# Optimization experiments

Measured on AMD Instinct MI355X. Metric: run time of the kernel, lower is better.

The kernel has to match this reference:

```python
import jax, jax.numpy as jnp
import numpy as np

D_MODEL = 1024
N_HEADS = 16
HEAD_DIM = D_MODEL // N_HEADS
ROPE_BASE = 10000.0


def _rope_cos_sin(t, dtype):
    # inv_freq over half the head dim, standard RoPE (GPT-NeoX style)
    inv_freq = 1.0 / (ROPE_BASE ** (jnp.arange(0, HEAD_DIM, 2, dtype=jnp.float32) / HEAD_DIM))
    freqs = jnp.arange(t, dtype=jnp.float32)[:, None] * inv_freq[None, :]  # [t, hd/2]
    emb = jnp.concatenate([freqs, freqs], axis=-1)  # [t, hd]
    return jnp.cos(emb).astype(dtype), jnp.sin(emb).astype(dtype)


def _rotate_half(x):
    x1, x2 = jnp.split(x, 2, axis=-1)
    return jnp.concatenate([-x2, x1], axis=-1)


def _apply_rope(x, cos, sin):
    # x: [b, h, t, hd]; cos/sin: [t, hd]
    return x * cos[None, None] + _rotate_half(x) * sin[None, None]


def setup_inputs() -> dict:
    key = jax.random.key(0)
    kx, kqkv, kout = jax.random.split(key, 3)
    x = jax.random.normal(kx, (4, 2048, D_MODEL), dtype=jnp.float32)
    scale = 1.0 / np.sqrt(D_MODEL)
    Wqkv = jax.random.normal(kqkv, (D_MODEL, 3 * D_MODEL), dtype=jnp.float32) * scale
    Wout = jax.random.normal(kout, (D_MODEL, D_MODEL), dtype=jnp.float32) * scale
    return {"x": x, "Wqkv": Wqkv, "Wout": Wout}


def reference(x, Wqkv, Wout):
    b, t, _ = x.shape
    qkv = (x @ Wqkv).reshape(b, t, 3, N_HEADS, HEAD_DIM)
    q, k, v = qkv[:, :, 0], qkv[:, :, 1], qkv[:, :, 2]  # [b, t, h, hd]
    q = q.transpose(0, 2, 1, 3)  # [b, h, t, hd]
    k = k.transpose(0, 2, 1, 3)
    v = v.transpose(0, 2, 1, 3)
    cos, sin = _rope_cos_sin(t, x.dtype)
    q = _apply_rope(q, cos, sin)
    k = _apply_rope(k, cos, sin)
    # causal SDPA
    scores = jnp.einsum("bhqd,bhkd->bhqk", q, k) / np.sqrt(HEAD_DIM)
    causal = jnp.tril(jnp.ones((t, t), dtype=bool))
    scores = jnp.where(causal[None, None], scores, jnp.finfo(scores.dtype).min)
    attn = jax.nn.softmax(scores, axis=-1)
    out = jnp.einsum("bhqk,bhkd->bhqd", attn, v)
    out = out.transpose(0, 2, 1, 3).reshape(b, t, D_MODEL)
    return out @ Wout
```

## Files before the change

### kernel.cpp

```cpp
#include <hip/hip_runtime.h>
#include <cstdint>
#include <cstddef>

typedef __bf16 bf16;
typedef __bf16 bf16x8 __attribute__((ext_vector_type(8)));
typedef __bf16 bf16x4 __attribute__((ext_vector_type(4)));
typedef float  f32x4  __attribute__((ext_vector_type(4)));
typedef float  f32x16 __attribute__((ext_vector_type(16)));

#define MFMA16(a, b, c) __builtin_amdgcn_mfma_f32_16x16x32_bf16((a), (b), (c), 0, 0, 0)
#define MFMA32(a, b, c) __builtin_amdgcn_mfma_f32_32x32x16_bf16((a), (b), (c), 0, 0, 0)

static constexpr int BB   = 4;
static constexpr int TT   = 2048;
static constexpr int DM   = 1024;
static constexpr int NH   = 16;
static constexpr int HD   = 64;
static constexpr int TOK  = BB * TT;
static constexpr int NQKV = 3 * DM;

__device__ inline void gload16(const void* g, void* l) {
    __builtin_amdgcn_global_load_lds((const __attribute__((address_space(1))) void*)g,
                                     (__attribute__((address_space(3))) void*)l, 16, 0, 0);
}

__device__ inline int swz(int x) { return x ^ ((x >> 3) & 0x70); }

__global__ void k_cvt(const float* __restrict__ in, bf16* __restrict__ out, int n) {
    int i = (blockIdx.x * blockDim.x + threadIdx.x) * 4;
    if (i >= n) return;
    float4 v = *(const float4*)(in + i);
    bf16x4 o;
    o[0] = (bf16)v.x; o[1] = (bf16)v.y; o[2] = (bf16)v.z; o[3] = (bf16)v.w;
    *(bf16x4*)(out + i) = o;
}

__global__ void k_transpose_cvt(const float* __restrict__ in, bf16* __restrict__ out,
                                int R, int C) {
    __shared__ bf16 tl[64 * 72];
    int tid = threadIdx.x;
    int c0 = blockIdx.x * 64, r0 = blockIdx.y * 64;
#pragma unroll
    for (int rep = 0; rep < 4; rep++) {
        int r = rep * 16 + (tid >> 4);
        int c = (tid & 15) * 4;
        float4 v = *(const float4*)(in + (size_t)(r0 + r) * C + c0 + c);
        tl[r * 72 + c + 0] = (bf16)v.x;
        tl[r * 72 + c + 1] = (bf16)v.y;
        tl[r * 72 + c + 2] = (bf16)v.z;
        tl[r * 72 + c + 3] = (bf16)v.w;
    }
    __syncthreads();
#pragma unroll
    for (int rep = 0; rep < 4; rep++) {
        int cc = rep * 16 + (tid >> 4);
        int rr = (tid & 15) * 4;
        bf16x4 o;
        o[0] = tl[(rr + 0) * 72 + cc];
        o[1] = tl[(rr + 1) * 72 + cc];
        o[2] = tl[(rr + 2) * 72 + cc];
        o[3] = tl[(rr + 3) * 72 + cc];
        *(bf16x4*)(out + (size_t)(c0 + cc) * R + r0 + rr) = o;
    }
}

__global__ void k_rope_tab(float* __restrict__ ct, float* __restrict__ st) {
    int i = blockIdx.x * blockDim.x + threadIdx.x;
    int t = i >> 5, j = i & 31;
    float invf = powf(10000.0f, -(float)j * (1.0f / 32.0f));
    float a = (float)t * invf;
    ct[i] = cosf(a);
    st[i] = sinf(a);
}

template <int MODE>
__global__ __launch_bounds__(256) void k_gemm_bt(
    const bf16* __restrict__ A, const bf16* __restrict__ Bt,
    int M, int N, int K,
    float* __restrict__ outF,
    bf16* __restrict__ qbuf, bf16* __restrict__ kbuf, bf16* __restrict__ vbuf,
    const float* __restrict__ ct, const float* __restrict__ st, float qscale) {
    __shared__ bf16 lA[128 * 64];
    __shared__ bf16 lB[128 * 64];
    int tid = threadIdx.x;
    int l = tid & 63, wid = tid >> 6;
    int wm = wid >> 1, wn = wid & 1;
    int bn = blockIdx.x, bm = blockIdx.y;
    const bf16* Ab = A + (size_t)bm * 128 * K;
    const bf16* Bb = Bt + (size_t)bn * 128 * K;
    int srow = l >> 3, scol = (l & 7) * 8;
    f32x4 acc[4][4] = {};
    for (int kt = 0; kt < K; kt += 64) {
        __syncthreads();
#pragma unroll
        for (int i = 0; i < 4; i++) {
            int chunk = wid * 4 + i;
            gload16(Ab + (size_t)(chunk * 8 + srow) * K + kt + scol, &lA[chunk * 512]);
            gload16(Bb + (size_t)(chunk * 8 + srow) * K + kt + scol, &lB[chunk * 512]);
        }
        __syncthreads();
#pragma unroll
        for (int kk = 0; kk < 2; kk++) {
            bf16x8 af[4], bfr[4];
#pragma unroll
            for (int mi = 0; mi < 4; mi++)
                af[mi] = *(const bf16x8*)&lA[(wm * 64 + mi * 16 + (l & 15)) * 64 + kk * 32 + (l >> 4) * 8];
#pragma unroll
            for (int ni = 0; ni < 4; ni++)
                bfr[ni] = *(const bf16x8*)&lB[(wn * 64 + ni * 16 + (l & 15)) * 64 + kk * 32 + (l >> 4) * 8];
#pragma unroll
            for (int mi = 0; mi < 4; mi++)
#pragma unroll
                for (int ni = 0; ni < 4; ni++)
                    acc[mi][ni] = MFMA16(af[mi], bfr[ni], acc[mi][ni]);
        }
    }
    if (MODE == 2) {
#pragma unroll
        for (int mi = 0; mi < 4; mi++) {
            int m0 = bm * 128 + wm * 64 + mi * 16 + ((l >> 4) << 2);
#pragma unroll
            for (int ni = 0; ni < 4; ni++) {
                int n = bn * 128 + wn * 64 + ni * 16 + (l & 15);
#pragma unroll
                for (int rj = 0; rj < 4; rj++)
                    outF[(size_t)(m0 + rj) * N + n] = acc[mi][ni][rj];
            }
        }
    } else {
        int n0 = bn * 128 + wn * 64;
        int sQ = n0 >> 10;
        int h = (n0 & 1023) >> 6;
        if (sQ == 2) {
#pragma unroll
            for (int ni = 0; ni < 4; ni++) {
                int d = ni * 16 + (l & 15);
#pragma unroll
                for (int mi = 0; mi < 4; mi++) {
                    int m0 = bm * 128 + wm * 64 + mi * 16 + ((l >> 4) << 2);
                    int b = m0 >> 11, t0 = m0 & 2047;
                    bf16x4 pv;
#pragma unroll
                    for (int rj = 0; rj < 4; rj++) pv[rj] = (bf16)acc[mi][ni][rj];
                    *(bf16x4*)(vbuf + ((size_t)((b * NH + h) * HD + d)) * TT + t0) = pv;
                }
            }
        } else {
            float qs = (sQ == 0) ? qscale : 1.0f;
            bf16* obuf = (sQ == 0) ? qbuf : kbuf;
#pragma unroll
            for (int mi = 0; mi < 4; mi++) {
                int m0 = bm * 128 + wm * 64 + mi * 16 + ((l >> 4) << 2);
                int b = m0 >> 11, t0 = m0 & 2047;
#pragma unroll
                for (int rj = 0; rj < 4; rj++) {
                    int t = t0 + rj;
                    bf16* dst = obuf + ((size_t)(b * NH + h) * TT + t) * HD;
                    const float* crow = ct + t * 32;
                    const float* srow = st + t * 32;
#pragma unroll
                    for (int ni2 = 0; ni2 < 2; ni2++) {
                        int d = ni2 * 16 + (l & 15);
                        float cs = crow[d], sn = srow[d];
                        float a  = acc[mi][ni2][rj];
                        float b2 = acc[mi][ni2 + 2][rj];
                        dst[d]      = (bf16)(qs * (a  * cs - b2 * sn));
                        dst[d + 32] = (bf16)(qs * (b2 * cs + a  * sn));
                    }
                }
            }
        }
    }
}

__global__ __launch_bounds__(256, 2) void k_attn(
    const bf16* __restrict__ Q, const bf16* __restrict__ K,
    const bf16* __restrict__ Vt, bf16* __restrict__ O) {
    __shared__ bf16 lK[2][4096];
    __shared__ bf16 lV[2][4096];
    __shared__ bf16 lP[8192];
    int tid = threadIdx.x;
    int l = tid & 63, w = tid >> 6;
    int bx = blockIdx.x, by = blockIdx.y;
    int bh = bx * 8 + (by >> 3);
    int p = by & 7;
    const char* KbB = (const char*)(K + (size_t)bh * TT * HD);
    const char* VbB = (const char*)(Vt + (size_t)bh * HD * TT);
    int b = bh >> 4, h = bh & 15;

    bf16x8 ones;
#pragma unroll
    for (int e = 0; e < 8; e++) ones[e] = (bf16)1.0f;

#define STAGE_KV(nb, j) do {                                                               \
    int X0_ = w * 1024 + l * 16;                                                           \
    const char* Kj_ = KbB + (size_t)(j) * 8192;                                            \
    gload16(Kj_ + swz(X0_),        (char*)lK[nb] + w * 1024);                              \
    gload16(Kj_ + swz(X0_ + 4096), (char*)lK[nb] + w * 1024 + 4096);                       \
    int o0_ = swz(X0_), o1_ = swz(X0_ + 4096);                                             \
    gload16(VbB + (size_t)(o0_ >> 7) * (TT * 2) + (size_t)(j) * 128 + (o0_ & 127),         \
            (char*)lV[nb] + w * 1024);                                                     \
    gload16(VbB + (size_t)(o1_ >> 7) * (TT * 2) + (size_t)(j) * 128 + (o1_ & 127),         \
            (char*)lV[nb] + w * 1024 + 4096);                                              \
} while (0)

    for (int half = 0; half < 2; half++) {
        int s = (half == 0) ? (15 - p) : p;
        int r0 = s * 128;
        int nblk = 2 * s + 2;
        int wrow = r0 + w * 32;
        const bf16* Qb = Q + ((size_t)bh * TT + wrow) * HD;
        bf16x8 qa[4];
#pragma unroll
        for (int kc = 0; kc < 4; kc++)
            qa[kc] = *(const bf16x8*)(Qb + (size_t)(l & 31) * HD + kc * 16 + (l >> 5) * 8);

        f32x16 oacc[2] = {};
        f32x16 lacc = {};

        STAGE_KV(0, 0);
        __syncthreads();
        int cur = 0;
        for (int j = 0; j < nblk; j++) {
            if (j + 1 < nblk) STAGE_KV(cur ^ 1, j + 1);
            if (j * 64 <= wrow + 31) {
                f32x16 sc[2];
#pragma unroll
                for (int r = 0; r < 16; r++) { sc[0][r] = -16.0f; sc[1][r] = -16.0f; }
                __builtin_amdgcn_s_setprio(1);
#pragma unroll
                for (int kc = 0; kc < 4; kc++)
#pragma unroll
                    for (int nj = 0; nj < 2; nj++) {
                        int rr = nj * 32 + (l & 31);
                        int L = rr * 128 + ((kc * 16 + (l >> 5) * 8) * 2 ^ ((rr & 7) << 4));
                        bf16x8 kb = *(const bf16x8*)((const char*)lK[cur] + L);
                        sc[nj] = MFMA32(qa[kc], kb, sc[nj]);
                    }
                __builtin_amdgcn_s_setprio(0);
                if (j * 64 + 63 > wrow) {
#pragma unroll
                    for (int nj = 0; nj < 2; nj++) {
                        int colg = j * 64 + nj * 32 + (l & 31);
#pragma unroll
                        for (int r = 0; r < 16; r++) {
                            int rowq = wrow + (r & 3) + 8 * (r >> 2) + 4 * (l >> 5);
                            if (colg > rowq) sc[nj][r] = -1e30f;
                        }
                    }
                }
                {
                    int prB = w * 32 + 4 * (l >> 5);
#pragma unroll
                    for (int nj = 0; nj < 2; nj++) {
                        int pcB = (nj * 32 + (l & 31)) * 2;
#pragma unroll
                        for (int r = 0; r < 16; r++) {
                            int row = prB + (r & 3) + 8 * (r >> 2);
                            *(bf16*)((char*)lP + row * 128 + (pcB ^ ((row & 7) << 4)))
                                = (bf16)exp2f(sc[nj][r]);
                        }
                    }
                }
                __builtin_amdgcn_s_setprio(1);
#pragma unroll
                for (int kc = 0; kc < 4; kc++) {
                    int pr = w * 32 + (l & 31);
                    bf16x8 pa = *(const bf16x8*)((const char*)lP + pr * 128
                                 + ((kc * 32 + (l >> 5) * 16) ^ ((pr & 7) << 4)));
                    lacc = MFMA32(pa, ones, lacc);
#pragma unroll
                    for (int dt = 0; dt < 2; dt++) {
                        int dd = dt * 32 + (l & 31);
                        int L = dd * 128 + ((kc * 16 + (l >> 5) * 8) * 2 ^ ((dd & 7) << 4));
                        bf16x8 vbf = *(const bf16x8*)((const char*)lV[cur] + L);
                        oacc[dt] = MFMA32(pa, vbf, oacc[dt]);
                    }
                }
                __builtin_amdgcn_s_setprio(0);
            }
            __syncthreads();
            cur ^= 1;
        }
#pragma unroll
        for (int r = 0; r < 16; r++) {
            int rq = (r & 3) + 8 * (r >> 2) + 4 * (l >> 5);
            int t = wrow + rq;
            float inv = 1.0f / lacc[r];
            size_t base = ((size_t)b * TT + t) * DM + h * HD;
#pragma unroll
            for (int dt = 0; dt < 2; dt++)
                O[base + dt * 32 + (l & 31)] = (bf16)(oacc[dt][r] * inv);
        }
    }
#undef STAGE_KV
}

extern "C" void kernel_launch(void* const* d_in, const int* in_sizes, int n_in,
                              void* d_out, int out_size, void* d_ws, size_t ws_size,
                              hipStream_t stream) {
    const float* x    = (const float*)d_in[0];
    const float* Wqkv = (const float*)d_in[1];
    const float* Wout = (const float*)d_in[2];
    float* out = (float*)d_out;

    char* ws = (char*)d_ws;
    size_t off = 0;
    auto alloc = [&](size_t bytes) {
        void* p = ws + off;
        off += (bytes + 255) & ~(size_t)255;
        return p;
    };
    bf16* xb    = (bf16*)alloc((size_t)TOK * DM * 2);
    bf16* wqkvt = (bf16*)alloc((size_t)NQKV * DM * 2);
    bf16* woutt = (bf16*)alloc((size_t)DM * DM * 2);
    bf16* qr    = (bf16*)alloc((size_t)TOK * DM * 2);
    bf16* kr    = (bf16*)alloc((size_t)TOK * DM * 2);
    bf16* vt    = (bf16*)alloc((size_t)TOK * DM * 2);
    bf16* ob    = (bf16*)alloc((size_t)TOK * DM * 2);
    float* ct   = (float*)alloc((size_t)TT * 32 * 4);
    float* st   = (float*)alloc((size_t)TT * 32 * 4);
    (void)ws_size; (void)in_sizes; (void)n_in; (void)out_size;

    k_cvt<<<TOK * DM / 4 / 256, 256, 0, stream>>>(x, xb, TOK * DM);
    k_transpose_cvt<<<dim3(NQKV / 64, DM / 64), 256, 0, stream>>>(Wqkv, wqkvt, DM, NQKV);
    k_transpose_cvt<<<dim3(DM / 64, DM / 64), 256, 0, stream>>>(Wout, woutt, DM, DM);
    k_rope_tab<<<TT * 32 / 256, 256, 0, stream>>>(ct, st);
    k_gemm_bt<1><<<dim3(NQKV / 128, TOK / 128), 256, 0, stream>>>(
        xb, wqkvt, TOK, NQKV, DM, nullptr, qr, kr, vt,
        ct, st, 0.125f * 1.4426950408889634f);
    k_attn<<<dim3(8, BB * NH), 256, 0, stream>>>(qr, kr, vt, ob);
    k_gemm_bt<2><<<dim3(DM / 128, TOK / 128), 256, 0, stream>>>(
        ob, woutt, TOK, DM, DM, out, nullptr, nullptr, nullptr,
        nullptr, nullptr, 0.0f);
}
```

Before: 206.0 us.

## Double-buffer GEMM LDS tiles and swizzle shared-memory layout

The projection GEMM kernel now keeps two LDS buffers for A and B, prefetching the next K tile with direct global-to-LDS loads while MFMAs run on the current tile, with one barrier per step. Tile placement in LDS uses a swizzled byte layout on both the load and read side to reduce bank conflicts on the fragment reads. This doubles the LDS footprint per block, which may lower occupancy.

```diff
diff --git a/kernel.cpp b/kernel.cpp
--- a/kernel.cpp
+++ b/kernel.cpp
@@ -80,41 +80,60 @@
     float* __restrict__ outF,
     bf16* __restrict__ qbuf, bf16* __restrict__ kbuf, bf16* __restrict__ vbuf,
     const float* __restrict__ ct, const float* __restrict__ st, float qscale) {
-    __shared__ bf16 lA[128 * 64];
-    __shared__ bf16 lB[128 * 64];
+    __shared__ bf16 lA[2][128 * 64];
+    __shared__ bf16 lB[2][128 * 64];
     int tid = threadIdx.x;
     int l = tid & 63, wid = tid >> 6;
     int wm = wid >> 1, wn = wid & 1;
     int bn = blockIdx.x, bm = blockIdx.y;
-    const bf16* Ab = A + (size_t)bm * 128 * K;
-    const bf16* Bb = Bt + (size_t)bn * 128 * K;
-    int srow = l >> 3, scol = (l & 7) * 8;
+    const char* AbB = (const char*)(A + (size_t)bm * 128 * K);
+    const char* BbB = (const char*)(Bt + (size_t)bn * 128 * K);
+    const size_t KB = (size_t)K * 2;
     f32x4 acc[4][4] = {};
-    for (int kt = 0; kt < K; kt += 64) {
-        __syncthreads();
-#pragma unroll
-        for (int i = 0; i < 4; i++) {
-            int chunk = wid * 4 + i;
-            gload16(Ab + (size_t)(chunk * 8 + srow) * K + kt + scol, &lA[chunk * 512]);
-            gload16(Bb + (size_t)(chunk * 8 + srow) * K + kt + scol, &lB[chunk * 512]);
-        }
-        __syncthreads();
+
+#define GSTAGE(nb, kt) do {                                                                \
+    _Pragma("unroll") for (int i = 0; i < 4; i++) {                                        \
+        int cb = (wid * 4 + i) * 1024;               \
+        int Xs = swz(cb + l * 16);                   \
+        gload16(AbB + (size_t)(Xs >> 7) * KB + (size_t)(kt) * 2 + (Xs & 127),              \
+                (char*)lA[nb] + cb);                                                       \
+        gload16(BbB + (size_t)(Xs >> 7) * KB + (size_t)(kt) * 2 + (Xs & 127),              \
+                (char*)lB[nb] + cb);                                                       \
+    }                                                                                      \
+} while (0)
+
+    GSTAGE(0, 0);
+    __syncthreads();
+    int cur = 0;
+    int nsteps = K >> 6;
+    for (int t = 0; t < nsteps; t++) {
+        if (t + 1 < nsteps) GSTAGE(cur ^ 1, (t + 1) << 6);
 #pragma unroll
         for (int kk = 0; kk < 2; kk++) {
             bf16x8 af[4], bfr[4];
 #pragma unroll
-            for (int mi = 0; mi < 4; mi++)
-                af[mi] = *(const bf16x8*)&lA[(wm * 64 + mi * 16 + (l & 15)) * 64 + kk * 32 + (l >> 4) * 8];
-#pragma unroll
-            for (int ni = 0; ni < 4; ni++)
-                bfr[ni] = *(const bf16x8*)&lB[(wn * 64 + ni * 16 + (l & 15)) * 64 + kk * 32 + (l >> 4) * 8];
+            for (int mi = 0; mi < 4; mi++) {
+                int rr = wm * 64 + mi * 16 + (l & 15);
+                int L = rr * 128 + (kk * 32 + (l >> 4) * 8) * 2;
+                af[mi] = *(const bf16x8*)((const char*)lA[cur] + swz(L));
+            }
+#pragma unroll
+            for (int ni = 0; ni < 4; ni++) {
+                int rr = wn * 64 + ni * 16 + (l & 15);
+                int L = rr * 128 + (kk * 32 + (l >> 4) * 8) * 2;
+                bfr[ni] = *(const bf16x8*)((const char*)lB[cur] + swz(L));
+            }
 #pragma unroll
             for (int mi = 0; mi < 4; mi++)
 #pragma unroll
                 for (int ni = 0; ni < 4; ni++)
                     acc[mi][ni] = MFMA16(af[mi], bfr[ni], acc[mi][ni]);
         }
-    }
+        __syncthreads();
+        cur ^= 1;
+    }
+#undef GSTAGE
+
     if (MODE == 2) {
 #pragma unroll
         for (int mi = 0; mi < 4; mi++) {
```

Result: faster. 189.0 us (-8.3%).
